# Performance work log

Hardware: AMD Instinct MI355X
Metric: run time of the kernel (lower is better)

The kernel has to match this reference:

```python
import jax, jax.numpy as jnp
import numpy as np

D, DC, DR, NH = 2048, 512, 64, 16
HD = D // NH
B, T = 2, 2048


def _rope_tables(sl, off, dr):
    inv = 1.0 / (10000.0 ** (jnp.arange(0, dr, 2, dtype=jnp.float32) / dr))
    t = jnp.arange(off, off + sl, dtype=jnp.float32)
    f = jnp.outer(t, inv)                      # [sl, dr/2]
    e = jnp.concatenate([f, f], -1)            # [sl, dr]
    return jnp.cos(e), jnp.sin(e)


def _rap(x, c, s):
    d = x.shape[-1]
    x1, x2 = x[..., : d // 2], x[..., d // 2:]
    ch, sh = c[..., : d // 2], s[..., : d // 2]
    return jnp.concatenate([x1 * ch - x2 * sh, x2 * ch + x1 * sh], -1)


def setup_inputs() -> dict:
    key = jax.random.key(0)
    ks = jax.random.split(key, 8)
    def w(k, i, o):
        return jax.random.normal(k, (i, o), jnp.float32) * (1.0 / np.sqrt(i))
    return {
        "x": jax.random.normal(ks[0], (B, T, D), jnp.float32),
        "Wkv": w(ks[1], D, DC),    # kv_down
        "Wkup": w(ks[2], DC, D),   # k_up
        "Wvup": w(ks[3], DC, D),   # v_up
        "Wq": w(ks[4], D, D),      # q_proj
        "Wqr": w(ks[5], D, DR),    # q_rope
        "Wkr": w(ks[6], DC, DR),   # k_rope
        "Wo": w(ks[7], D, D),      # o_proj
    }


def reference(x, Wkv, Wkup, Wvup, Wq, Wqr, Wkr, Wo):
    Bx, Tx, d = x.shape
    offset = 0
    ckv = x @ Wkv                                   # [B,T,dc]
    kr = ckv @ Wkr                                  # [B,T,dr]
    cos, sin = _rope_tables(Tx, offset, DR)         # [T,dr]
    kr = _rap(kr, cos[None], sin[None])
    entry = jnp.concatenate([ckv, kr], -1)          # [B,T,dc+dr] (kv cache entry)
    tl = entry.shape[1]

    k = (ckv @ Wkup).reshape(Bx, tl, NH, HD).transpose(0, 2, 1, 3)   # [B,H,tl,hd]
    v = (ckv @ Wvup).reshape(Bx, tl, NH, HD).transpose(0, 2, 1, 3)
    q = (x @ Wq).reshape(Bx, Tx, NH, HD).transpose(0, 2, 1, 3)        # [B,H,T,hd]

    qr = _rap(x @ Wqr, cos[None], sin[None])        # [B,T,dr]

    ac = jnp.einsum("bhtd,bhsd->bhts", q, k)        # content scores
    ar = jnp.einsum("btd,bsd->bts", qr, kr)         # shared RoPE scores (same per head)
    scale = np.sqrt(HD + DR).astype(np.float32)
    scores = (ac + ar[:, None]) / scale             # [B,H,T,tl]

    # causal mask: triu(-inf, diagonal=tl-T+1)
    i = jnp.arange(Tx)[:, None]
    j = jnp.arange(tl)[None, :]
    mask = j > i + (tl - Tx)
    scores = jnp.where(mask[None, None], -jnp.inf, scores)

    attn = jax.nn.softmax(scores, -1)
    out = jnp.einsum("bhts,bhsd->bhtd", attn, v).transpose(0, 2, 1, 3).reshape(Bx, Tx, -1)
    return out @ Wo, entry
```

## Files before the change

### kernel.cpp

```cpp
#include <hip/hip_runtime.h>
#include <math.h>
#include <type_traits>

#define D    2048
#define DC   512
#define DR   64
#define NH   16
#define HD   128
#define Bb   2
#define Tt   2048
#define ROWS (Bb*Tt)
#define LDX  2176

typedef __bf16 bf16x8 __attribute__((ext_vector_type(8)));
typedef __bf16 bf16x4 __attribute__((ext_vector_type(4)));
typedef float  f32x4  __attribute__((ext_vector_type(4)));

typedef const void __attribute__((address_space(1))) gvoid;
typedef void       __attribute__((address_space(3))) lvoid;

__device__ __forceinline__ void load_lds16(const void* g, void* l) {
    __builtin_amdgcn_global_load_lds((gvoid*)g, (lvoid*)l, 16, 0, 0);
}

template <bool WF32, bool WBF16>
__global__ __launch_bounds__(256)
void gemm_bt(const __bf16* __restrict__ A, const __bf16* __restrict__ BT,
             float* __restrict__ Cf, __bf16* __restrict__ Cb,
             int M, int K, int ldcf, int ldcb) {
    __shared__ __bf16 As[128 * 32];
    __shared__ __bf16 Bs[128 * 32];

    const int tid  = threadIdx.x;
    const int w    = tid >> 6;
    const int lane = tid & 63;
    const int quad = lane >> 4;
    const int lc   = lane & 15;
    const int bm   = blockIdx.y * 128;
    const int bn   = blockIdx.x * 128;
    const int wm   = (w & 1) * 64;
    const int wn   = (w >> 1) * 64;

    const int sr = w * 32 + (lane >> 2);
    const int sc = (lane & 3) * 8;

    f32x4 acc[4][4] = {};

    for (int k0 = 0; k0 < K; k0 += 32) {
        const __bf16* ga = A  + (size_t)(bm + sr) * K + k0 + sc;
        const __bf16* gb = BT + (size_t)(bn + sr) * K + k0 + sc;
        load_lds16(ga,                  &As[(w * 32) * 32]);
        load_lds16(ga + (size_t)16 * K, &As[(w * 32 + 16) * 32]);
        load_lds16(gb,                  &Bs[(w * 32) * 32]);
        load_lds16(gb + (size_t)16 * K, &Bs[(w * 32 + 16) * 32]);
        __syncthreads();

        bf16x8 af[4], bfr[4];
        #pragma unroll
        for (int mi = 0; mi < 4; ++mi)
            af[mi] = *(bf16x8*)&As[(wm + mi * 16 + lc) * 32 + quad * 8];
        #pragma unroll
        for (int ni = 0; ni < 4; ++ni)
            bfr[ni] = *(bf16x8*)&Bs[(wn + ni * 16 + lc) * 32 + quad * 8];
        #pragma unroll
        for (int mi = 0; mi < 4; ++mi)
            #pragma unroll
            for (int ni = 0; ni < 4; ++ni)
                acc[mi][ni] = __builtin_amdgcn_mfma_f32_16x16x32_bf16(
                    af[mi], bfr[ni], acc[mi][ni], 0, 0, 0);
        __syncthreads();
    }

    #pragma unroll
    for (int mi = 0; mi < 4; ++mi)
        #pragma unroll
        for (int r = 0; r < 4; ++r) {
            const int row = bm + wm + mi * 16 + quad * 4 + r;
            const int col = bn + wn + lc;
            #pragma unroll
            for (int ni = 0; ni < 4; ++ni) {
                float v = acc[mi][ni][r];
                if constexpr (WF32)  Cf[(size_t)row * ldcf + col + ni * 16] = v;
                if constexpr (WBF16) Cb[(size_t)row * ldcb + col + ni * 16] = (__bf16)v;
            }
        }
}

__global__ void f32_to_bf16(const float* __restrict__ in,
                            __bf16* __restrict__ out, int n) {
    int i = blockIdx.x * blockDim.x + threadIdx.x;
    if (i < n) out[i] = (__bf16)in[i];
}

__global__ __launch_bounds__(256)
void transpose_conv(const float* __restrict__ W, __bf16* __restrict__ WT,
                    int R, int C) {
    __shared__ float tile[64][65];
    const int r0 = blockIdx.x * 64;
    const int c0 = blockIdx.y * 64;
    const int tid = threadIdx.x;
    for (int e = tid; e < 64 * 64; e += 256) {
        int i = e >> 6, j = e & 63;
        tile[i][j] = W[(size_t)(r0 + i) * C + c0 + j];
    }
    __syncthreads();
    for (int e = tid; e < 64 * 64; e += 256) {
        int i = e >> 6, j = e & 63;
        WT[(size_t)(c0 + i) * R + r0 + j] = (__bf16)tile[j][i];
    }
}

__global__ void rope_ext(__bf16* __restrict__ p, float* __restrict__ ent) {
    int idx = blockIdx.x * blockDim.x + threadIdx.x;
    if (idx >= ROWS * 32) return;
    int row = idx >> 5;
    int i   = idx & 31;
    int t   = row & (Tt - 1);
    float inv  = powf(10000.0f, -(float)(2 * i) / 64.0f);
    float fr   = (float)t * inv;
    float c = cosf(fr), s = sinf(fr);
    __bf16* v = p + (size_t)row * LDX + 2048;
    float x1 = (float)v[i], x2 = (float)v[i + 32];
    float o1 = x1 * c - x2 * s;
    float o2 = x2 * c + x1 * s;
    v[i]      = (__bf16)o1;
    v[i + 32] = (__bf16)o2;
    if (ent) {
        ent[(size_t)row * 576 + 512 + i] = o1;
        ent[(size_t)row * 576 + 544 + i] = o2;
    }
}

__global__ __launch_bounds__(256)
void transpose_v(const __bf16* __restrict__ vb, __bf16* __restrict__ vtb) {
    __shared__ __bf16 tile[64][65];
    const int t0 = blockIdx.x * 64;
    const int c0 = blockIdx.y * 64;
    const int b  = blockIdx.z;
    const int tid = threadIdx.x;
    for (int e = tid; e < 64 * 64; e += 256) {
        int i = e >> 6, j = e & 63;
        tile[i][j] = vb[((size_t)(b * Tt + t0 + i)) * D + c0 + j];
    }
    __syncthreads();
    for (int e = tid; e < 64 * 64; e += 256) {
        int i = e >> 6, j = e & 63;
        vtb[((size_t)(b * D + c0 + i)) * Tt + t0 + j] = tile[j][i];
    }
}

#define KS_STR 200
#define VT_STR 72
#define PS_STR 72
#define SPLIT_TILES 8

__device__ __forceinline__ int pbase_qt(int qt) {
    int a = qt >> 3, r = qt & 7;
    return qt + 4 * a * (a - 1) + a * r;
}

__global__ __launch_bounds__(256, 3)
void attn_split(const __bf16* __restrict__ qx, const __bf16* __restrict__ kx,
                const __bf16* __restrict__ vtb, __bf16* __restrict__ opart,
                float* __restrict__ mlpart) {
    const int qt = (Tt / 64 - 1) - (int)blockIdx.y;
    const int sp = blockIdx.x;
    const int t0 = sp * SPLIT_TILES;
    if (t0 > qt) return;
    const int tend = min(t0 + SPLIT_TILES, qt + 1);
    const int hb = blockIdx.z;
    const int h  = hb & (NH - 1);
    const int b  = hb >> 4;
    const int q0 = qt * 64;

    __shared__ __bf16 Ks[64][KS_STR];
    __shared__ __bf16 Vt[128][VT_STR];
    __shared__ __bf16 PsT[4][16][PS_STR];

    const int tid  = threadIdx.x;
    const int w    = tid >> 6;
    const int lane = tid & 63;
    const int quad = lane >> 4;
    const int lc   = lane & 15;

    bf16x8 aq[6];
    {
        const __bf16* qrow = qx + (size_t)(b * Tt + q0 + w * 16 + lc) * LDX;
        #pragma unroll
        for (int kt = 0; kt < 4; ++kt)
            aq[kt] = *(const bf16x8*)(qrow + h * HD + kt * 32 + quad * 8);
        #pragma unroll
        for (int kt = 0; kt < 2; ++kt)
            aq[4 + kt] = *(const bf16x8*)(qrow + 2048 + kt * 32 + quad * 8);
    }

    int krow[6], kcol[6], kgo[6];
    #pragma unroll
    for (int j = 0; j < 6; ++j) {
        int c   = tid + j * 256;
        int row = c / 24, c24 = c - row * 24;
        krow[j] = row;
        kcol[j] = c24 * 8;
        kgo[j]  = row * LDX + ((c24 < 16) ? (h * HD + c24 * 8)
                                          : (2048 + (c24 - 16) * 8));
    }
    const int vrow = tid >> 3;
    const int vcol = (tid & 7) * 8;
    const __bf16* kb0 = kx + (size_t)b * Tt * LDX;
    const __bf16* vb0 = vtb + ((size_t)b * D + (size_t)h * HD) * Tt;

    bf16x8 pk[6], pvv[4];
    {
        const __bf16* kbt = kb0 + (size_t)(t0 * 64) * LDX;
        const __bf16* vbt = vb0 + t0 * 64;
        #pragma unroll
        for (int j = 0; j < 6; ++j) pk[j] = *(const bf16x8*)(kbt + kgo[j]);
        #pragma unroll
        for (int j = 0; j < 4; ++j)
            pvv[j] = *(const bf16x8*)(vbt + (vrow + j * 32) * Tt + vcol);
    }

    float m_i = -1e30f, l_i = 0.f;
    f32x4 Of[8];
    #pragma unroll
    for (int n = 0; n < 8; ++n) Of[n] = (f32x4){0.f, 0.f, 0.f, 0.f};

    const float rscale = 0.07216878364870323f;
    const int qglob = q0 + w * 16 + lc;

    for (int it = t0; it < tend; ++it) {
        const int s0 = it * 64;
        __syncthreads();
        #pragma unroll
        for (int j = 0; j < 6; ++j) *(bf16x8*)&Ks[krow[j]][kcol[j]] = pk[j];
        #pragma unroll
        for (int j = 0; j < 4; ++j) *(bf16x8*)&Vt[vrow + j * 32][vcol] = pvv[j];
        __syncthreads();

        if (it + 1 < tend) {
            const __bf16* kbn = kb0 + (size_t)(s0 + 64) * LDX;
            const __bf16* vbn = vb0 + (s0 + 64);
            #pragma unroll
            for (int j = 0; j < 6; ++j) pk[j] = *(const bf16x8*)(kbn + kgo[j]);
            #pragma unroll
            for (int j = 0; j < 4; ++j)
                pvv[j] = *(const bf16x8*)(vbn + (vrow + j * 32) * Tt + vcol);
        }

        f32x4 st[4];
        #pragma unroll
        for (int f = 0; f < 4; ++f) st[f] = (f32x4){0.f, 0.f, 0.f, 0.f};
        #pragma unroll
        for (int kt = 0; kt < 6; ++kt) {
            #pragma unroll
            for (int f = 0; f < 4; ++f) {
                bf16x8 ak = *(bf16x8*)&Ks[f * 16 + lc][kt * 32 + quad * 8];
                st[f] = __builtin_amdgcn_mfma_f32_16x16x32_bf16(ak, aq[kt], st[f], 0, 0, 0);
            }
        }

        const bool dm = (it == qt);
        float mt = -1e30f;
        #pragma unroll
        for (int f = 0; f < 4; ++f)
            #pragma unroll
            for (int r = 0; r < 4; ++r) {
                float sv = st[f][r] * rscale;
                if (dm && (s0 + f * 16 + quad * 4 + r > qglob)) sv = -1e30f;
                st[f][r] = sv;
                mt = fmaxf(mt, sv);
            }
        mt = fmaxf(mt, __shfl_xor(mt, 16, 64));
        mt = fmaxf(mt, __shfl_xor(mt, 32, 64));
        float mn = fmaxf(m_i, mt);
        float al = __expf(m_i - mn);
        m_i = mn;
        float rsum = 0.f;
        #pragma unroll
        for (int f = 0; f < 4; ++f) {
            bf16x4 pr;
            #pragma unroll
            for (int r = 0; r < 4; ++r) {
                __bf16 pb = (__bf16)__expf(st[f][r] - mn);
                pr[r] = pb;
                rsum += (float)pb;
            }
            *(bf16x4*)&PsT[w][lc][f * 16 + quad * 4] = pr;
        }
        rsum += __shfl_xor(rsum, 16, 64);
        rsum += __shfl_xor(rsum, 32, 64);
        l_i = l_i * al + rsum;
        #pragma unroll
        for (int n = 0; n < 8; ++n)
            #pragma unroll
            for (int r = 0; r < 4; ++r) Of[n][r] *= al;

        #pragma unroll
        for (int kt = 0; kt < 2; ++kt) {
            bf16x8 bp = *(bf16x8*)&PsT[w][lc][kt * 32 + quad * 8];
            #pragma unroll
            for (int n = 0; n < 8; ++n) {
                bf16x8 av = *(bf16x8*)&Vt[n * 16 + lc][kt * 32 + quad * 8];
                Of[n] = __builtin_amdgcn_mfma_f32_16x16x32_bf16(av, bp, Of[n], 0, 0, 0);
            }
        }
    }

    const int p = hb * 80 + pbase_qt(qt) + sp;
    __bf16* ob = opart + (size_t)p * (64 * 128) + (size_t)(w * 16 + lc) * 128;
    #pragma unroll
    for (int n = 0; n < 8; ++n) {
        bf16x4 o4;
        #pragma unroll
        for (int r = 0; r < 4; ++r) o4[r] = (__bf16)Of[n][r];
        *(bf16x4*)(ob + n * 16 + quad * 4) = o4;
    }
    if (quad == 0) {
        mlpart[(size_t)p * 128 + w * 16 + lc]      = m_i;
        mlpart[(size_t)p * 128 + 64 + w * 16 + lc] = l_i;
    }
}

__global__ __launch_bounds__(256)
void attn_reduce(const __bf16* __restrict__ opart, const float* __restrict__ mlpart,
                 __bf16* __restrict__ aob) {
    const int qt = blockIdx.x;
    const int hb = blockIdx.y;
    const int h  = hb & (NH - 1);
    const int b  = hb >> 4;
    const int nsp = (qt >> 3) + 1;
    const int p0  = hb * 80 + pbase_qt(qt);
    const int tid = threadIdx.x;
    const int ql  = tid >> 2;
    const int cg  = (tid & 3) * 32;

    float M = -1e30f;
    for (int s = 0; s < nsp; ++s)
        M = fmaxf(M, mlpart[(size_t)(p0 + s) * 128 + ql]);
    float L = 0.f;
    float acc[32];
    #pragma unroll
    for (int j = 0; j < 32; ++j) acc[j] = 0.f;
    for (int s = 0; s < nsp; ++s) {
        float ms = mlpart[(size_t)(p0 + s) * 128 + ql];
        float ls = mlpart[(size_t)(p0 + s) * 128 + 64 + ql];
        float sc = __expf(ms - M);
        L += ls * sc;
        const __bf16* op = opart + (size_t)(p0 + s) * (64 * 128) + (size_t)ql * 128 + cg;
        #pragma unroll
        for (int j8 = 0; j8 < 4; ++j8) {
            bf16x8 v = *(const bf16x8*)(op + j8 * 8);
            #pragma unroll
            for (int e = 0; e < 8; ++e) acc[j8 * 8 + e] += sc * (float)v[e];
        }
    }
    float invL = 1.0f / L;
    __bf16* outp = aob + ((size_t)(b * Tt + qt * 64 + ql)) * D + h * HD + cg;
    #pragma unroll
    for (int j8 = 0; j8 < 4; ++j8) {
        bf16x8 v;
        #pragma unroll
        for (int e = 0; e < 8; ++e) v[e] = (__bf16)(acc[j8 * 8 + e] * invL);
        *(bf16x8*)(outp + j8 * 8) = v;
    }
}

extern "C" void kernel_launch(void* const* d_in, const int* in_sizes, int n_in,
                              void* d_out, int out_size, void* d_ws, size_t ws_size,
                              hipStream_t stream) {
    const float* x    = (const float*)d_in[0];
    const float* Wkv  = (const float*)d_in[1];
    const float* Wkup = (const float*)d_in[2];
    const float* Wvup = (const float*)d_in[3];
    const float* Wq   = (const float*)d_in[4];
    const float* Wqr  = (const float*)d_in[5];
    const float* Wkr  = (const float*)d_in[6];
    const float* Wo   = (const float*)d_in[7];

    float* out0 = (float*)d_out;
    float* out1 = out0 + (size_t)ROWS * D;

    char* wsb = (char*)d_ws;
    __bf16* qext = (__bf16*)wsb;  wsb += (size_t)ROWS * LDX * 2;
    __bf16* kext = (__bf16*)wsb;  wsb += (size_t)ROWS * LDX * 2;
    __bf16* vtb  = (__bf16*)wsb;  wsb += (size_t)ROWS * D   * 2;
    __bf16* aob  = (__bf16*)wsb;  wsb += (size_t)ROWS * D   * 2;
    __bf16* WoT  = (__bf16*)wsb;  wsb += (size_t)D * D * 2;

    char* scratch = wsb;
    __bf16* xb    = (__bf16*)scratch;
    __bf16* vb    = (__bf16*)(scratch + 16777216);
    __bf16* ckvb  = (__bf16*)(scratch + 33554432);
    __bf16* WkvT  = (__bf16*)(scratch + 37748736);
    __bf16* WqxT  = (__bf16*)(scratch + 39845888);
    __bf16* KupxT = (__bf16*)(scratch + 48758784);
    __bf16* WvupT = (__bf16*)(scratch + 50987008);
    __bf16* opart  = (__bf16*)scratch;
    float*  mlpart = (float*)(scratch + (size_t)2560 * 64 * 128 * 2);

    dim3 blk(256);

    f32_to_bf16<<<(ROWS * D + 255) / 256, blk, 0, stream>>>(x, xb, ROWS * D);
    transpose_conv<<<dim3(D / 64, DC / 64), blk, 0, stream>>>(Wkv, WkvT, D, DC);
    transpose_conv<<<dim3(D / 64, D / 64),  blk, 0, stream>>>(Wq, WqxT, D, D);
    transpose_conv<<<dim3(D / 64, 1),       blk, 0, stream>>>(Wqr, WqxT + (size_t)D * D, D, DR);
    transpose_conv<<<dim3(DC / 64, D / 64), blk, 0, stream>>>(Wkup, KupxT, DC, D);
    transpose_conv<<<dim3(DC / 64, 1),      blk, 0, stream>>>(Wkr, KupxT + (size_t)D * DC, DC, DR);
    transpose_conv<<<dim3(DC / 64, D / 64), blk, 0, stream>>>(Wvup, WvupT, DC, D);
    transpose_conv<<<dim3(D / 64, D / 64),  blk, 0, stream>>>(Wo, WoT, D, D);

    gemm_bt<true, true><<<dim3(DC / 128, ROWS / 128), blk, 0, stream>>>(
        xb, WkvT, out1, ckvb, ROWS, D, 576, DC);

    gemm_bt<false, true><<<dim3(LDX / 128, ROWS / 128), blk, 0, stream>>>(
        xb, WqxT, (float*)nullptr, qext, ROWS, D, 0, LDX);
    rope_ext<<<(ROWS * 32 + 255) / 256, blk, 0, stream>>>(qext, (float*)nullptr);

    gemm_bt<false, true><<<dim3(LDX / 128, ROWS / 128), blk, 0, stream>>>(
        ckvb, KupxT, (float*)nullptr, kext, ROWS, DC, 0, LDX);
    rope_ext<<<(ROWS * 32 + 255) / 256, blk, 0, stream>>>(kext, out1);

    gemm_bt<false, true><<<dim3(D / 128, ROWS / 128), blk, 0, stream>>>(
        ckvb, WvupT, (float*)nullptr, vb, ROWS, DC, 0, D);
    transpose_v<<<dim3(Tt / 64, D / 64, Bb), blk, 0, stream>>>(vb, vtb);

    attn_split<<<dim3(4, Tt / 64, NH * Bb), blk, 0, stream>>>(
        qext, kext, vtb, opart, mlpart);
    attn_reduce<<<dim3(Tt / 64, NH * Bb), blk, 0, stream>>>(opart, mlpart, aob);

    gemm_bt<true, false><<<dim3(D / 128, ROWS / 128), blk, 0, stream>>>(
        aob, WoT, out0, (__bf16*)nullptr, ROWS, D, D, 0);
}
```

Measured before the change: 552.6 us.

## Process two query tiles per attention block to reuse K/V loads, use exp2 softmax

Each attention block now handles a 128-row query pair instead of 64 rows, so every K/V tile staged in LDS feeds two query sub-tiles. This halves K/V global traffic and the staging syncs per query row. The softmax now uses exp2 with the scale folded in, and the two RoPE launches are merged into one kernel. In exchange the kernel holds twice the accumulators in registers, so the occupancy hint drops from 3 to 2 blocks per SM. Causal work is also less balanced, because the lower query tile computes on a diagonal block that is fully masked.

Result: slower. 745.0 us (+34.8%).

```diff
diff --git a/kernel.cpp b/kernel.cpp
--- a/kernel.cpp
+++ b/kernel.cpp
@@ -110,22 +110,25 @@
     }
 }
 
-__global__ void rope_ext(__bf16* __restrict__ p, float* __restrict__ ent) {
+__global__ void rope_both(__bf16* __restrict__ qx, __bf16* __restrict__ kx,
+                          float* __restrict__ ent) {
     int idx = blockIdx.x * blockDim.x + threadIdx.x;
-    if (idx >= ROWS * 32) return;
-    int row = idx >> 5;
-    int i   = idx & 31;
+    if (idx >= 2 * ROWS * 32) return;
+    int sel = idx >= ROWS * 32;
+    int id2 = idx - sel * ROWS * 32;
+    int row = id2 >> 5;
+    int i   = id2 & 31;
     int t   = row & (Tt - 1);
     float inv  = powf(10000.0f, -(float)(2 * i) / 64.0f);
     float fr   = (float)t * inv;
     float c = cosf(fr), s = sinf(fr);
-    __bf16* v = p + (size_t)row * LDX + 2048;
+    __bf16* v = (sel ? kx : qx) + (size_t)row * LDX + 2048;
     float x1 = (float)v[i], x2 = (float)v[i + 32];
     float o1 = x1 * c - x2 * s;
     float o2 = x2 * c + x1 * s;
     v[i]      = (__bf16)o1;
     v[i + 32] = (__bf16)o2;
-    if (ent) {
+    if (sel) {
         ent[(size_t)row * 576 + 512 + i] = o1;
         ent[(size_t)row * 576 + 544 + i] = o2;
     }
@@ -159,23 +162,24 @@
     return qt + 4 * a * (a - 1) + a * r;
 }
 
-__global__ __launch_bounds__(256, 3)
+__global__ __launch_bounds__(256, 2)
 void attn_split(const __bf16* __restrict__ qx, const __bf16* __restrict__ kx,
                 const __bf16* __restrict__ vtb, __bf16* __restrict__ opart,
                 float* __restrict__ mlpart) {
-    const int qt = (Tt / 64 - 1) - (int)blockIdx.y;
-    const int sp = blockIdx.x;
-    const int t0 = sp * SPLIT_TILES;
-    if (t0 > qt) return;
-    const int tend = min(t0 + SPLIT_TILES, qt + 1);
+    const int qp  = 15 - (int)blockIdx.y;
+    const int qth = 2 * qp + 1;
+    const int sp  = blockIdx.x;
+    const int t0  = sp * SPLIT_TILES;
+    if (t0 > qth) return;
+    const int tend = min(t0 + SPLIT_TILES, qth + 1);
     const int hb = blockIdx.z;
     const int h  = hb & (NH - 1);
     const int b  = hb >> 4;
-    const int q0 = qt * 64;
+    const int q0 = qp * 128;
 
     __shared__ __bf16 Ks[64][KS_STR];
     __shared__ __bf16 Vt[128][VT_STR];
-    __shared__ __bf16 PsT[4][16][PS_STR];
+    __shared__ __bf16 PsT[2][4][16][PS_STR];
 
     const int tid  = threadIdx.x;
     const int w    = tid >> 6;
@@ -183,15 +187,16 @@
     const int quad = lane >> 4;
     const int lc   = lane & 15;
 
-    bf16x8 aq[6];
-    {
-        const __bf16* qrow = qx + (size_t)(b * Tt + q0 + w * 16 + lc) * LDX;
+    bf16x8 aq[2][6];
+    #pragma unroll
+    for (int qs = 0; qs < 2; ++qs) {
+        const __bf16* qrow = qx + (size_t)(b * Tt + q0 + qs * 64 + w * 16 + lc) * LDX;
         #pragma unroll
         for (int kt = 0; kt < 4; ++kt)
-            aq[kt] = *(const bf16x8*)(qrow + h * HD + kt * 32 + quad * 8);
+            aq[qs][kt] = *(const bf16x8*)(qrow + h * HD + kt * 32 + quad * 8);
         #pragma unroll
         for (int kt = 0; kt < 2; ++kt)
-            aq[4 + kt] = *(const bf16x8*)(qrow + 2048 + kt * 32 + quad * 8);
+            aq[qs][4 + kt] = *(const bf16x8*)(qrow + 2048 + kt * 32 + quad * 8);
     }
 
     int krow[6], kcol[6], kgo[6];
@@ -220,13 +225,15 @@
             pvv[j] = *(const bf16x8*)(vbt + (vrow + j * 32) * Tt + vcol);
     }
 
-    float m_i = -1e30f, l_i = 0.f;
-    f32x4 Of[8];
-    #pragma unroll
-    for (int n = 0; n < 8; ++n) Of[n] = (f32x4){0.f, 0.f, 0.f, 0.f};
+    float m_i[2] = {-1e30f, -1e30f}, l_i[2] = {0.f, 0.f};
+    f32x4 Of[2][8];
+    #pragma unroll
+    for (int qs = 0; qs < 2; ++qs)
+        #pragma unroll
+        for (int n = 0; n < 8; ++n) Of[qs][n] = (f32x4){0.f, 0.f, 0.f, 0.f};
 
     const float rscale = 0.07216878364870323f;
-    const int qglob = q0 + w * 16 + lc;
+    const float RL2    = 0.10412413954269697f;
 
     for (int it = t0; it < tend; ++it) {
         const int s0 = it * 64;
@@ -247,77 +254,87 @@
                 pvv[j] = *(const bf16x8*)(vbn + (vrow + j * 32) * Tt + vcol);
         }
 
-        f32x4 st[4];
-        #pragma unroll
-        for (int f = 0; f < 4; ++f) st[f] = (f32x4){0.f, 0.f, 0.f, 0.f};
-        #pragma unroll
-        for (int kt = 0; kt < 6; ++kt) {
+        #pragma unroll
+        for (int qs = 0; qs < 2; ++qs) {
+            const int qglob = q0 + qs * 64 + w * 16 + lc;
+            f32x4 st[4];
+            #pragma unroll
+            for (int f = 0; f < 4; ++f) st[f] = (f32x4){0.f, 0.f, 0.f, 0.f};
+            #pragma unroll
+            for (int kt = 0; kt < 6; ++kt) {
+                #pragma unroll
+                for (int f = 0; f < 4; ++f) {
+                    bf16x8 ak = *(bf16x8*)&Ks[f * 16 + lc][kt * 32 + quad * 8];
+                    st[f] = __builtin_amdgcn_mfma_f32_16x16x32_bf16(
+                        ak, aq[qs][kt], st[f], 0, 0, 0);
+                }
+            }
+
+            const bool dm = (it >= 2 * qp + qs);
+            float mt = -1e30f;
+            #pragma unroll
+            for (int f = 0; f < 4; ++f)
+                #pragma unroll
+                for (int r = 0; r < 4; ++r) {
+                    float sv = st[f][r];
+                    if (dm && (s0 + f * 16 + quad * 4 + r > qglob)) sv = -1e30f;
+                    st[f][r] = sv;
+                    mt = fmaxf(mt, sv);
+                }
+            mt = fmaxf(mt, __shfl_xor(mt, 16, 64));
+            mt = fmaxf(mt, __shfl_xor(mt, 32, 64));
+            float mn  = fmaxf(m_i[qs], mt);
+            float al  = __builtin_amdgcn_exp2f((m_i[qs] - mn) * RL2);
+            m_i[qs]   = mn;
+            float mnl = mn * RL2;
+            float rsum = 0.f;
             #pragma unroll
             for (int f = 0; f < 4; ++f) {
-                bf16x8 ak = *(bf16x8*)&Ks[f * 16 + lc][kt * 32 + quad * 8];
-                st[f] = __builtin_amdgcn_mfma_f32_16x16x32_bf16(ak, aq[kt], st[f], 0, 0, 0);
+                bf16x4 pr;
+                #pragma unroll
+                for (int r = 0; r < 4; ++r) {
+                    float p = __builtin_amdgcn_exp2f(fmaf(st[f][r], RL2, -mnl));
+                    pr[r] = (__bf16)p;
+                    rsum += p;
+                }
+                *(bf16x4*)&PsT[qs][w][lc][f * 16 + quad * 4] = pr;
             }
-        }
-
-        const bool dm = (it == qt);
-        float mt = -1e30f;
-        #pragma unroll
-        for (int f = 0; f < 4; ++f)
-            #pragma unroll
-            for (int r = 0; r < 4; ++r) {
-                float sv = st[f][r] * rscale;
-                if (dm && (s0 + f * 16 + quad * 4 + r > qglob)) sv = -1e30f;
-                st[f][r] = sv;
-                mt = fmaxf(mt, sv);
+            rsum += __shfl_xor(rsum, 16, 64);
+            rsum += __shfl_xor(rsum, 32, 64);
+            l_i[qs] = l_i[qs] * al + rsum;
+            #pragma unroll
+            for (int n = 0; n < 8; ++n)
+                #pragma unroll
+                for (int r = 0; r < 4; ++r) Of[qs][n][r] *= al;
+
+            #pragma unroll
+            for (int kt = 0; kt < 2; ++kt) {
+                bf16x8 bp = *(bf16x8*)&PsT[qs][w][lc][kt * 32 + quad * 8];
+                #pragma unroll
+                for (int n = 0; n < 8; ++n) {
+                    bf16x8 av = *(bf16x8*)&Vt[n * 16 + lc][kt * 32 + quad * 8];
+                    Of[qs][n] = __builtin_amdgcn_mfma_f32_16x16x32_bf16(
+                        av, bp, Of[qs][n], 0, 0, 0);
+                }
             }
-        mt = fmaxf(mt, __shfl_xor(mt, 16, 64));
-        mt = fmaxf(mt, __shfl_xor(mt, 32, 64));
-        float mn = fmaxf(m_i, mt);
-        float al = __expf(m_i - mn);
-        m_i = mn;
-        float rsum = 0.f;
-        #pragma unroll
-        for (int f = 0; f < 4; ++f) {
-            bf16x4 pr;
-            #pragma unroll
-            for (int r = 0; r < 4; ++r) {
-                __bf16 pb = (__bf16)__expf(st[f][r] - mn);
-                pr[r] = pb;
-                rsum += (float)pb;
-            }
-            *(bf16x4*)&PsT[w][lc][f * 16 + quad * 4] = pr;
-        }
-        rsum += __shfl_xor(rsum, 16, 64);
-        rsum += __shfl_xor(rsum, 32, 64);
-        l_i = l_i * al + rsum;
-        #pragma unroll
-        for (int n = 0; n < 8; ++n)
-            #pragma unroll
-            for (int r = 0; r < 4; ++r) Of[n][r] *= al;
-
-        #pragma unroll
-        for (int kt = 0; kt < 2; ++kt) {
-            bf16x8 bp = *(bf16x8*)&PsT[w][lc][kt * 32 + quad * 8];
-            #pragma unroll
-            for (int n = 0; n < 8; ++n) {
-                bf16x8 av = *(bf16x8*)&Vt[n * 16 + lc][kt * 32 + quad * 8];
-                Of[n] = __builtin_amdgcn_mfma_f32_16x16x32_bf16(av, bp, Of[n], 0, 0, 0);
-            }
-        }
-    }
-
-    const int p = hb * 80 + pbase_qt(qt) + sp;
-    __bf16* ob = opart + (size_t)p * (64 * 128) + (size_t)(w * 16 + lc) * 128;
-    #pragma unroll
-    for (int n = 0; n < 8; ++n) {
-        bf16x4 o4;
-        #pragma unroll
-        for (int r = 0; r < 4; ++r) o4[r] = (__bf16)Of[n][r];
-        *(bf16x4*)(ob + n * 16 + quad * 4) = o4;
-    }
-    if (quad == 0) {
-        mlpart[(size_t)p * 128 + w * 16 + lc]      = m_i;
-        mlpart[(size_t)p * 128 + 64 + w * 16 + lc] = l_i;
+        }
+    }
+
+    #pragma unroll
+    for (int qs = 0; qs < 2; ++qs) {
+        const int p = hb * 80 + pbase_qt(2 * qp + qs) + sp;
+        __bf16* ob = opart + (size_t)p * (64 * 128) + (size_t)(w * 16 + lc) * 128;
+        #pragma unroll
+        for (int n = 0; n < 8; ++n) {
+            bf16x4 o4;
+            #pragma unroll
+            for (int r = 0; r < 4; ++r) o4[r] = (__bf16)Of[qs][n][r];
+            *(bf16x4*)(ob + n * 16 + quad * 4) = o4;
+        }
+        if (quad == 0) {
+            mlpart[(size_t)p * 128 + w * 16 + lc]      = m_i[qs] * rscale;
+            mlpart[(size_t)p * 128 + 64 + w * 16 + lc] = l_i[qs];
+        }
     }
 }
 
@@ -414,17 +431,15 @@
 
     gemm_bt<false, true><<<dim3(LDX / 128, ROWS / 128), blk, 0, stream>>>(
         xb, WqxT, (float*)nullptr, qext, ROWS, D, 0, LDX);
-    rope_ext<<<(ROWS * 32 + 255) / 256, blk, 0, stream>>>(qext, (float*)nullptr);
-
     gemm_bt<false, true><<<dim3(LDX / 128, ROWS / 128), blk, 0, stream>>>(
         ckvb, KupxT, (float*)nullptr, kext, ROWS, DC, 0, LDX);
-    rope_ext<<<(ROWS * 32 + 255) / 256, blk, 0, stream>>>(kext, out1);
+    rope_both<<<(2 * ROWS * 32 + 255) / 256, blk, 0, stream>>>(qext, kext, out1);
 
     gemm_bt<false, true><<<dim3(D / 128, ROWS / 128), blk, 0, stream>>>(
         ckvb, WvupT, (float*)nullptr, vb, ROWS, DC, 0, D);
     transpose_v<<<dim3(Tt / 64, D / 64, Bb), blk, 0, stream>>>(vb, vtb);
 
-    attn_split<<<dim3(4, Tt / 64, NH * Bb), blk, 0, stream>>>(
+    attn_split<<<dim3(4, Tt / 128, NH * Bb), blk, 0, stream>>>(
         qext, kext, vtb, opart, mlpart);
     attn_reduce<<<dim3(Tt / 64, NH * Bb), blk, 0, stream>>>(opart, mlpart, aob);
 
```
